# Kernel optimization log

Measured on AMD Instinct MI355X. Metric: run time of the kernel, lower is better.

The kernel has to match this reference:

```python
import jax, jax.numpy as jnp
import numpy as np

N_NODES = 20000
N_GRAPHS = 8
NODES_PER_GRAPH = N_NODES // N_GRAPHS
DEG = 16
N_EDGES = N_NODES * DEG
D = 128
MAX_ITER = 8
HISTORY = 5
LAM = 0.1
LN_EPS = 1e-5


def setup_inputs() -> dict:
    key = jax.random.key(0)
    k1, k2, k3, k4, k5 = jax.random.split(key, 5)
    # edges constrained to stay within each graph's node block
    src = jax.random.randint(k1, (N_EDGES,), 0, N_NODES, dtype=jnp.int32)
    offs = (src // NODES_PER_GRAPH) * NODES_PER_GRAPH
    dst = offs + jax.random.randint(k2, (N_EDGES,), 0, NODES_PER_GRAPH, dtype=jnp.int32)
    # scale values ~1/deg so the fixed-point map stays well-behaved
    sparse_values = jax.random.normal(k3, (N_EDGES,), dtype=jnp.float32) * (1.0 / DEG)
    return {
        "x_init": jax.random.normal(k4, (N_NODES, D), dtype=jnp.float32),
        "norm_K_diag": jax.random.uniform(k5, (N_NODES, 1), dtype=jnp.float32),
        "sparse_values": sparse_values,
        "ln_w": jnp.ones((D,), dtype=jnp.float32),
        "ln_b": jnp.zeros((D,), dtype=jnp.float32),
        "edge_rows": src,
        "edge_cols": dst,
        "batch": jnp.repeat(jnp.arange(N_GRAPHS, dtype=jnp.int32), NODES_PER_GRAPH),
        "max_iter": MAX_ITER,
    }


def _spmm(vals, rows, cols, z):
    # sparse COO matmul: out[r] += vals_e * z[cols_e]; coalesce-equivalent since
    # segment_sum adds duplicate indices.
    return jax.ops.segment_sum(vals[:, None] * z[cols], rows, num_segments=N_NODES)


def _layernorm(x, w, b):
    mu = jnp.mean(x, axis=-1, keepdims=True)
    var = jnp.mean((x - mu) ** 2, axis=-1, keepdims=True)
    return w * (x - mu) * jax.lax.rsqrt(var + LN_EPS) + b


def reference(x_init, norm_K_diag, sparse_values, ln_w, ln_b, edge_rows, edge_cols, batch, max_iter):
    def f(z):
        out = norm_K_diag * z + _spmm(sparse_values, edge_rows, edge_cols, z)
        return _layernorm(out, ln_w, ln_b)

    z = x_init
    z_hist, f_hist = [], []
    for i in range(max_iter):  # fixed, small unroll (DEQ max_iter)
        f_z = f(z)
        z_hist.append(z.reshape(-1))
        f_hist.append(f_z.reshape(-1))
        if len(z_hist) > HISTORY:
            z_hist.pop(0)
            f_hist.pop(0)
        if len(z_hist) > 1 and i > 5:
            Z = jnp.stack(z_hist, axis=1)   # [N*D, h]
            F = jnp.stack(f_hist, axis=1)
            G = F - Z
            dG = G[:, 1:] - G[:, :-1]
            dF = F[:, 1:] - F[:, :-1]
            H = dG.T @ dG + LAM * jnp.eye(dG.shape[1], dtype=z.dtype)
            gamma = jnp.linalg.solve(H, dG.T @ G[:, -1:])
            z_new = (F[:, -1:] - dF @ gamma).reshape(z.shape)
            z = jnp.where(jnp.all(jnp.isfinite(z_new)), 0.5 * f_z + 0.5 * z_new, f_z)
        else:
            z = f_z
    return z
```

## Files before the change

kernel.cpp:

```cpp
#include <hip/hip_runtime.h>
#include <math.h>

#define N_NODES 20000
#define N_EDGES 320000
#define DD 128
#define ND (N_NODES * DD)
#define ND4 (ND / 4)
#define NPG 2500


__global__ void count_kernel(const int* __restrict__ rows, int* __restrict__ cnt) {
    int e = blockIdx.x * blockDim.x + threadIdx.x;
    if (e < N_EDGES) atomicAdd(&cnt[rows[e]], 1);
}

__global__ __launch_bounds__(1024) void scan_kernel(const int* __restrict__ cnt,
                                                    int* __restrict__ row_start,
                                                    int* __restrict__ cursor,
                                                    float* __restrict__ redz) {
    const int t = threadIdx.x;
    if (t < 448) redz[t] = 0.0f;
    __shared__ int part[1024];
    const int CH = (N_NODES + 1023) / 1024;
    int lo = t * CH, hi = min(lo + CH, N_NODES);
    int s = 0;
    for (int i = lo; i < hi; ++i) s += cnt[i];
    part[t] = s;
    __syncthreads();
    for (int off = 1; off < 1024; off <<= 1) {
        int v = (t >= off) ? part[t - off] : 0;
        __syncthreads();
        if (t >= off) part[t] += v;
        __syncthreads();
    }
    int run = (t > 0) ? part[t - 1] : 0;
    for (int i = lo; i < hi; ++i) {
        row_start[i] = run;
        cursor[i] = run;
        run += cnt[i];
    }
    if (t == 1023) row_start[N_NODES] = part[1023];
}

__global__ void scatter_kernel(const int* __restrict__ rows, const int* __restrict__ cols,
                               const float* __restrict__ vals, int* __restrict__ cursor,
                               float2* __restrict__ epack) {
    int e = blockIdx.x * blockDim.x + threadIdx.x;
    if (e >= N_EDGES) return;
    int r = rows[e];
    int p = atomicAdd(&cursor[r], 1);
    epack[p] = make_float2(vals[e], __int_as_float(cols[e]));
}


__global__ __launch_bounds__(128) void feval_kernel(const float* __restrict__ z,
                                                    const float* __restrict__ Kd,
                                                    const float* __restrict__ lnw,
                                                    const float* __restrict__ lnb,
                                                    const int* __restrict__ row_start,
                                                    const float2* __restrict__ epack,
                                                    float* __restrict__ out) {
    int b = blockIdx.x;
    int g = b & 7;
    int j = b >> 3;
    int wv = threadIdx.x >> 6;
    int lane = threadIdx.x & 63;
    int l = lane & 31;
    int r = g * NPG + (j << 2) + (wv << 1) + (lane >> 5);
    int d0 = l << 2;

    float4 zv = *(const float4*)(z + (size_t)r * DD + d0);
    float kd = Kd[r];
    float a0 = kd * zv.x, a1 = kd * zv.y, a2 = kd * zv.z, a3 = kd * zv.w;

    int e0 = row_start[r], e1 = row_start[r + 1];
    for (int base = e0; base < e1; base += 32) {
        int ew = base + l;
        float2 my_e = (ew < e1) ? epack[ew] : make_float2(0.0f, 0.0f);
        float my_val = my_e.x;
        int my_col = __float_as_int(my_e.y);
        int m = min(32, e1 - base);
        int i = 0;
        for (; i + 4 <= m; i += 4) {
            int c0 = __shfl(my_col, i, 32);
            int c1 = __shfl(my_col, i + 1, 32);
            int c2 = __shfl(my_col, i + 2, 32);
            int c3 = __shfl(my_col, i + 3, 32);
            float v0 = __shfl(my_val, i, 32);
            float v1 = __shfl(my_val, i + 1, 32);
            float v2 = __shfl(my_val, i + 2, 32);
            float v3 = __shfl(my_val, i + 3, 32);
            float4 z0 = *(const float4*)(z + (size_t)c0 * DD + d0);
            float4 z1 = *(const float4*)(z + (size_t)c1 * DD + d0);
            float4 z2 = *(const float4*)(z + (size_t)c2 * DD + d0);
            float4 z3 = *(const float4*)(z + (size_t)c3 * DD + d0);
            a0 = fmaf(v0, z0.x, a0); a1 = fmaf(v0, z0.y, a1); a2 = fmaf(v0, z0.z, a2); a3 = fmaf(v0, z0.w, a3);
            a0 = fmaf(v1, z1.x, a0); a1 = fmaf(v1, z1.y, a1); a2 = fmaf(v1, z1.z, a2); a3 = fmaf(v1, z1.w, a3);
            a0 = fmaf(v2, z2.x, a0); a1 = fmaf(v2, z2.y, a1); a2 = fmaf(v2, z2.z, a2); a3 = fmaf(v2, z2.w, a3);
            a0 = fmaf(v3, z3.x, a0); a1 = fmaf(v3, z3.y, a1); a2 = fmaf(v3, z3.z, a2); a3 = fmaf(v3, z3.w, a3);
        }
        for (; i < m; ++i) {
            int c = __shfl(my_col, i, 32);
            float v = __shfl(my_val, i, 32);
            float4 zc = *(const float4*)(z + (size_t)c * DD + d0);
            a0 = fmaf(v, zc.x, a0); a1 = fmaf(v, zc.y, a1);
            a2 = fmaf(v, zc.z, a2); a3 = fmaf(v, zc.w, a3);
        }
    }

    float s = a0 + a1 + a2 + a3;
    float sq = a0 * a0 + a1 * a1 + a2 * a2 + a3 * a3;
#pragma unroll
    for (int off = 16; off; off >>= 1) {
        s += __shfl_xor(s, off, 64);
        sq += __shfl_xor(sq, off, 64);
    }
    float mu = s * (1.0f / DD);
    float var = sq * (1.0f / DD) - mu * mu;
    float rstd = rsqrtf(var + 1e-5f);

    float4 wv4 = *(const float4*)(lnw + d0);
    float4 bv4 = *(const float4*)(lnb + d0);
    float4 ov;
    ov.x = wv4.x * (a0 - mu) * rstd + bv4.x;
    ov.y = wv4.y * (a1 - mu) * rstd + bv4.y;
    ov.z = wv4.z * (a2 - mu) * rstd + bv4.z;
    ov.w = wv4.w * (a3 - mu) * rstd + bv4.w;
    *(float4*)(out + (size_t)r * DD + d0) = ov;
}


struct Slots { const float* s[6]; const float* zlast; };
struct Cols5 { const float* f[5]; };

__device__ __forceinline__ float dot4(float4 a, float4 b) {
    return a.x * b.x + a.y * b.y + a.z * b.z + a.w * b.w;
}
__device__ __forceinline__ float4 sub4(float4 a, float4 b) {
    return make_float4(a.x - b.x, a.y - b.y, a.z - b.z, a.w - b.w);
}

#define RED_T 160000
__global__ __launch_bounds__(256) void reduce_kernel(Slots sl, float* __restrict__ red) {
    int tid = blockIdx.x * 256 + threadIdx.x;
    float acc[14];
#pragma unroll
    for (int k = 0; k < 14; ++k) acc[k] = 0.f;

#pragma unroll
    for (int ph = 0; ph < 2; ++ph) {
        int ja = tid + (2 * ph) * RED_T;
        int jb = ja + RED_T;
        float4 fa[6], fb[6];
#pragma unroll
        for (int c = 0; c < 6; ++c) {
            fa[c] = ((const float4*)sl.s[c])[ja];
            fb[c] = ((const float4*)sl.s[c])[jb];
        }
        float4 zla = ((const float4*)sl.zlast)[ja];
        float4 zlb = ((const float4*)sl.zlast)[jb];
        float4 Ga[5], Gb[5];
#pragma unroll
        for (int c = 0; c < 4; ++c) { Ga[c] = sub4(fa[c + 1], fa[c]); Gb[c] = sub4(fb[c + 1], fb[c]); }
        Ga[4] = sub4(fa[5], zla);
        Gb[4] = sub4(fb[5], zlb);
        float4 dga[4], dgb[4];
#pragma unroll
        for (int a = 0; a < 4; ++a) { dga[a] = sub4(Ga[a + 1], Ga[a]); dgb[a] = sub4(Gb[a + 1], Gb[a]); }
        int k = 0;
#pragma unroll
        for (int a = 0; a < 4; ++a)
#pragma unroll
            for (int b = a; b < 4; ++b) { acc[k] += dot4(dga[a], dga[b]) + dot4(dgb[a], dgb[b]); ++k; }
#pragma unroll
        for (int a = 0; a < 4; ++a) acc[10 + a] += dot4(dga[a], Ga[4]) + dot4(dgb[a], Gb[4]);
    }

#pragma unroll
    for (int off = 32; off; off >>= 1)
#pragma unroll
        for (int kk = 0; kk < 14; ++kk) acc[kk] += __shfl_xor(acc[kk], off, 64);

    __shared__ float sh[4][14];
    int wave = threadIdx.x >> 6, lane = threadIdx.x & 63;
    if (lane == 0)
#pragma unroll
        for (int kk = 0; kk < 14; ++kk) sh[wave][kk] = acc[kk];
    __syncthreads();
    if (threadIdx.x < 14) {
        int kk = threadIdx.x;
        atomicAdd(&red[kk * 16], sh[0][kk] + sh[1][kk] + sh[2][kk] + sh[3][kk]);
    }
}

__global__ void solve_kernel(const float* __restrict__ red, float* __restrict__ gam) {
    if (threadIdx.x != 0 || blockIdx.x != 0) return;
    float A[4][4], b[4];
    int k = 0;
    for (int a = 0; a < 4; ++a)
        for (int c = a; c < 4; ++c) { A[a][c] = red[k * 16]; A[c][a] = red[k * 16]; ++k; }
    for (int a = 0; a < 4; ++a) A[a][a] += 0.1f;
    for (int a = 0; a < 4; ++a) b[a] = red[(10 + a) * 16];

    for (int col = 0; col < 4; ++col) {
        int piv = col;
        float best = fabsf(A[col][col]);
        for (int rr = col + 1; rr < 4; ++rr) {
            float m = fabsf(A[rr][col]);
            if (m > best) { best = m; piv = rr; }
        }
        if (piv != col) {
            for (int c2 = 0; c2 < 4; ++c2) { float t = A[col][c2]; A[col][c2] = A[piv][c2]; A[piv][c2] = t; }
            float t = b[col]; b[col] = b[piv]; b[piv] = t;
        }
        float inv = 1.0f / A[col][col];
        for (int rr = col + 1; rr < 4; ++rr) {
            float m = A[rr][col] * inv;
            for (int c2 = col; c2 < 4; ++c2) A[rr][c2] -= m * A[col][c2];
            b[rr] -= m * b[col];
        }
    }
    float g[4];
    for (int rr = 3; rr >= 0; --rr) {
        float s = b[rr];
        for (int c2 = rr + 1; c2 < 4; ++c2) s -= A[rr][c2] * g[c2];
        g[rr] = s / A[rr][rr];
    }
    bool fin = isfinite(g[0]) && isfinite(g[1]) && isfinite(g[2]) && isfinite(g[3]);
    gam[0] = g[0]; gam[1] = g[1]; gam[2] = g[2]; gam[3] = g[3];
    gam[4] = fin ? 1.0f : 0.0f;
}

__global__ __launch_bounds__(256) void update_kernel(Cols5 c, const float* __restrict__ gam,
                                                     float* __restrict__ zout) {
    int j = blockIdx.x * blockDim.x + threadIdx.x;
    if (j >= ND4) return;
    float g0 = gam[0], g1 = gam[1], g2 = gam[2], g3 = gam[3], flag = gam[4];
    float4 f0 = ((const float4*)c.f[0])[j];
    float4 f1 = ((const float4*)c.f[1])[j];
    float4 f2 = ((const float4*)c.f[2])[j];
    float4 f3 = ((const float4*)c.f[3])[j];
    float4 f4 = ((const float4*)c.f[4])[j];
    float4 o;
    if (flag != 0.0f) {
        o.x = f4.x - 0.5f * ((f1.x - f0.x) * g0 + (f2.x - f1.x) * g1 + (f3.x - f2.x) * g2 + (f4.x - f3.x) * g3);
        o.y = f4.y - 0.5f * ((f1.y - f0.y) * g0 + (f2.y - f1.y) * g1 + (f3.y - f2.y) * g2 + (f4.y - f3.y) * g3);
        o.z = f4.z - 0.5f * ((f1.z - f0.z) * g0 + (f2.z - f1.z) * g1 + (f3.z - f2.z) * g2 + (f4.z - f3.z) * g3);
        o.w = f4.w - 0.5f * ((f1.w - f0.w) * g0 + (f2.w - f1.w) * g1 + (f3.w - f2.w) * g2 + (f4.w - f3.w) * g3);
    } else {
        o = f4;
    }
    ((float4*)zout)[j] = o;
}


extern "C" void kernel_launch(void* const* d_in, const int* in_sizes, int n_in,
                              void* d_out, int out_size, void* d_ws, size_t ws_size,
                              hipStream_t stream) {
    const float* x_init = (const float*)d_in[0];
    const float* Kd     = (const float*)d_in[1];
    const float* vals   = (const float*)d_in[2];
    const float* lnw    = (const float*)d_in[3];
    const float* lnb    = (const float*)d_in[4];
    const int*   rows   = (const int*)d_in[5];
    const int*   cols   = (const int*)d_in[6];
    float* out = (float*)d_out;

    char* p = (char*)d_ws;
    auto carve = [&](size_t bytes) -> void* {
        void* r = (void*)p;
        p += (bytes + 255) & ~(size_t)255;
        return r;
    };
    float*  Fh        = (float*)carve((size_t)6 * ND * 4);
    float*  red       = (float*)carve(4096);
    float*  gam       = (float*)carve(256);
    int*    row_start = (int*)carve((N_NODES + 1) * 4);
    int*    cursor    = (int*)carve(N_NODES * 4);
    int*    cnt       = (int*)carve(N_NODES * 4);
    float2* epack     = (float2*)carve((size_t)N_EDGES * 8);
    float*  zA        = out;

    hipMemsetAsync(cnt, 0, N_NODES * 4, stream);
    count_kernel<<<(N_EDGES + 255) / 256, 256, 0, stream>>>(rows, cnt);
    scan_kernel<<<1, 1024, 0, stream>>>(cnt, row_start, cursor, red);
    scatter_kernel<<<(N_EDGES + 255) / 256, 256, 0, stream>>>(rows, cols, vals, cursor, epack);

    auto Fslot = [&](int t) -> float* { return Fh + (size_t)(t % 6) * ND; };

    for (int t = 0; t < 8; ++t) {
        const float* zsrc = (t == 0) ? x_init : (t <= 6 ? Fslot(t - 1) : zA);
        feval_kernel<<<5000, 128, 0, stream>>>(zsrc, Kd, lnw, lnb, row_start, epack, Fslot(t));

        if (t >= 6) {
            float* redt = red + (t - 6) * 224;
            Slots sl;
            for (int i = 0; i < 6; ++i) sl.s[i] = Fslot(t - 5 + i);
            sl.zlast = (t == 7) ? (const float*)zA : (const float*)Fslot(t - 1);
            reduce_kernel<<<625, 256, 0, stream>>>(sl, redt);
            solve_kernel<<<1, 64, 0, stream>>>(redt, gam);

            Cols5 uc;
            for (int c2 = 0; c2 < 5; ++c2) uc.f[c2] = Fslot(t - 4 + c2);
            float* zdst = (t == 6) ? zA : out;
            update_kernel<<<(ND4 + 255) / 256, 256, 0, stream>>>(uc, gam, zdst);
        }
    }
}
```

Baseline: 306.8 us.

## Fuse 4x4 gamma solve into update kernel and unroll gather by eight

Drops the single-thread solve kernel and has every thread of the update kernel redundantly solve the small 4x4 system, removing two kernel launches and their serialization gaps. Pivoting is removed and the solve is fully unrolled so it stays in registers. The SpMM gather loop is unrolled from 4 to 8 edges so more independent row loads are in flight, and the row_start load is hoisted ahead of the self-row load. Dropping pivoting risks numerical differences, and the redundant per-thread solve adds ALU work and 14 broadcast loads per thread.

```diff
diff --git a/kernel.cpp b/kernel.cpp
--- a/kernel.cpp
+++ b/kernel.cpp
@@ -69,11 +69,12 @@
     int r = g * NPG + (j << 2) + (wv << 1) + (lane >> 5);
     int d0 = l << 2;
 
+    int e0 = row_start[r], e1 = row_start[r + 1];
+
     float4 zv = *(const float4*)(z + (size_t)r * DD + d0);
     float kd = Kd[r];
     float a0 = kd * zv.x, a1 = kd * zv.y, a2 = kd * zv.z, a3 = kd * zv.w;
 
-    int e0 = row_start[r], e1 = row_start[r + 1];
     for (int base = e0; base < e1; base += 32) {
         int ew = base + l;
         float2 my_e = (ew < e1) ? epack[ew] : make_float2(0.0f, 0.0f);
@@ -81,23 +82,21 @@
         int my_col = __float_as_int(my_e.y);
         int m = min(32, e1 - base);
         int i = 0;
-        for (; i + 4 <= m; i += 4) {
-            int c0 = __shfl(my_col, i, 32);
-            int c1 = __shfl(my_col, i + 1, 32);
-            int c2 = __shfl(my_col, i + 2, 32);
-            int c3 = __shfl(my_col, i + 3, 32);
-            float v0 = __shfl(my_val, i, 32);
-            float v1 = __shfl(my_val, i + 1, 32);
-            float v2 = __shfl(my_val, i + 2, 32);
-            float v3 = __shfl(my_val, i + 3, 32);
-            float4 z0 = *(const float4*)(z + (size_t)c0 * DD + d0);
-            float4 z1 = *(const float4*)(z + (size_t)c1 * DD + d0);
-            float4 z2 = *(const float4*)(z + (size_t)c2 * DD + d0);
-            float4 z3 = *(const float4*)(z + (size_t)c3 * DD + d0);
-            a0 = fmaf(v0, z0.x, a0); a1 = fmaf(v0, z0.y, a1); a2 = fmaf(v0, z0.z, a2); a3 = fmaf(v0, z0.w, a3);
-            a0 = fmaf(v1, z1.x, a0); a1 = fmaf(v1, z1.y, a1); a2 = fmaf(v1, z1.z, a2); a3 = fmaf(v1, z1.w, a3);
-            a0 = fmaf(v2, z2.x, a0); a1 = fmaf(v2, z2.y, a1); a2 = fmaf(v2, z2.z, a2); a3 = fmaf(v2, z2.w, a3);
-            a0 = fmaf(v3, z3.x, a0); a1 = fmaf(v3, z3.y, a1); a2 = fmaf(v3, z3.z, a2); a3 = fmaf(v3, z3.w, a3);
+        for (; i + 8 <= m; i += 8) {
+            int c[8]; float v[8];
+#pragma unroll
+            for (int u = 0; u < 8; ++u) {
+                c[u] = __shfl(my_col, i + u, 32);
+                v[u] = __shfl(my_val, i + u, 32);
+            }
+            float4 zr[8];
+#pragma unroll
+            for (int u = 0; u < 8; ++u) zr[u] = *(const float4*)(z + (size_t)c[u] * DD + d0);
+#pragma unroll
+            for (int u = 0; u < 8; ++u) {
+                a0 = fmaf(v[u], zr[u].x, a0); a1 = fmaf(v[u], zr[u].y, a1);
+                a2 = fmaf(v[u], zr[u].z, a2); a3 = fmaf(v[u], zr[u].w, a3);
+            }
         }
         for (; i < m; ++i) {
             int c = __shfl(my_col, i, 32);
@@ -193,49 +192,55 @@
     }
 }
 
-__global__ void solve_kernel(const float* __restrict__ red, float* __restrict__ gam) {
-    if (threadIdx.x != 0 || blockIdx.x != 0) return;
+__device__ __forceinline__ float solve_gamma(const float* __restrict__ red, float* g) {
     float A[4][4], b[4];
     int k = 0;
+#pragma unroll
     for (int a = 0; a < 4; ++a)
-        for (int c = a; c < 4; ++c) { A[a][c] = red[k * 16]; A[c][a] = red[k * 16]; ++k; }
+#pragma unroll
+        for (int c = 0; c < 4; ++c) A[a][c] = 0.f;
+#pragma unroll
+    for (int a = 0; a < 4; ++a)
+#pragma unroll
+        for (int c = a; c < 4; ++c) { float h = red[k * 16]; A[a][c] = h; A[c][a] = h; ++k; }
+#pragma unroll
     for (int a = 0; a < 4; ++a) A[a][a] += 0.1f;
+#pragma unroll
     for (int a = 0; a < 4; ++a) b[a] = red[(10 + a) * 16];
 
+#pragma unroll
     for (int col = 0; col < 4; ++col) {
-        int piv = col;
-        float best = fabsf(A[col][col]);
-        for (int rr = col + 1; rr < 4; ++rr) {
-            float m = fabsf(A[rr][col]);
-            if (m > best) { best = m; piv = rr; }
-        }
-        if (piv != col) {
-            for (int c2 = 0; c2 < 4; ++c2) { float t = A[col][c2]; A[col][c2] = A[piv][c2]; A[piv][c2] = t; }
-            float t = b[col]; b[col] = b[piv]; b[piv] = t;
-        }
         float inv = 1.0f / A[col][col];
-        for (int rr = col + 1; rr < 4; ++rr) {
-            float m = A[rr][col] * inv;
-            for (int c2 = col; c2 < 4; ++c2) A[rr][c2] -= m * A[col][c2];
-            b[rr] -= m * b[col];
-        }
-    }
-    float g[4];
+#pragma unroll
+        for (int rr = 0; rr < 4; ++rr) {
+            if (rr > col) {
+                float m = A[rr][col] * inv;
+#pragma unroll
+                for (int c2 = 0; c2 < 4; ++c2)
+                    if (c2 >= col) A[rr][c2] -= m * A[col][c2];
+                b[rr] -= m * b[col];
+            }
+        }
+    }
+#pragma unroll
     for (int rr = 3; rr >= 0; --rr) {
         float s = b[rr];
-        for (int c2 = rr + 1; c2 < 4; ++c2) s -= A[rr][c2] * g[c2];
+#pragma unroll
+        for (int c2 = 0; c2 < 4; ++c2)
+            if (c2 > rr) s -= A[rr][c2] * g[c2];
         g[rr] = s / A[rr][rr];
     }
     bool fin = isfinite(g[0]) && isfinite(g[1]) && isfinite(g[2]) && isfinite(g[3]);
-    gam[0] = g[0]; gam[1] = g[1]; gam[2] = g[2]; gam[3] = g[3];
-    gam[4] = fin ? 1.0f : 0.0f;
-}
-
-__global__ __launch_bounds__(256) void update_kernel(Cols5 c, const float* __restrict__ gam,
+    return fin ? 1.0f : 0.0f;
+}
+
+__global__ __launch_bounds__(256) void update_kernel(Cols5 c, const float* __restrict__ red,
                                                      float* __restrict__ zout) {
     int j = blockIdx.x * blockDim.x + threadIdx.x;
     if (j >= ND4) return;
-    float g0 = gam[0], g1 = gam[1], g2 = gam[2], g3 = gam[3], flag = gam[4];
+    float g[4];
+    float flag = solve_gamma(red, g);
+    float g0 = g[0], g1 = g[1], g2 = g[2], g3 = g[3];
     float4 f0 = ((const float4*)c.f[0])[j];
     float4 f1 = ((const float4*)c.f[1])[j];
     float4 f2 = ((const float4*)c.f[2])[j];
@@ -274,7 +279,6 @@
     };
     float*  Fh        = (float*)carve((size_t)6 * ND * 4);
     float*  red       = (float*)carve(4096);
-    float*  gam       = (float*)carve(256);
     int*    row_start = (int*)carve((N_NODES + 1) * 4);
     int*    cursor    = (int*)carve(N_NODES * 4);
     int*    cnt       = (int*)carve(N_NODES * 4);
@@ -298,12 +302,11 @@
             for (int i = 0; i < 6; ++i) sl.s[i] = Fslot(t - 5 + i);
             sl.zlast = (t == 7) ? (const float*)zA : (const float*)Fslot(t - 1);
             reduce_kernel<<<625, 256, 0, stream>>>(sl, redt);
-            solve_kernel<<<1, 64, 0, stream>>>(redt, gam);
 
             Cols5 uc;
             for (int c2 = 0; c2 < 5; ++c2) uc.f[c2] = Fslot(t - 4 + c2);
             float* zdst = (t == 6) ? zA : out;
-            update_kernel<<<(ND4 + 255) / 256, 256, 0, stream>>>(uc, gam, zdst);
-        }
-    }
-}
+            update_kernel<<<(ND4 + 255) / 256, 256, 0, stream>>>(uc, redt, zdst);
+        }
+    }
+}
```

Result: no change. 306.2 us (-0.2%).
